# Optimization experiments

Hardware: AMD Instinct MI355X
Metric: run time of the kernel (lower is better)

The kernel has to match this reference:

```python
import jax, jax.numpy as jnp
import numpy as np

N, C, H, W = 64, 64, 8, 8   # batch, channels (img_net_out_dim), feature-map HxW
E = 256                      # ques_rnn_hidden_dim
G = 512                      # rn_g_dim
FD = 512                     # rn_f_dim
GIN = 2 * (C + 2) + E        # g-MLP input dim = 388
NUM_CLASSES = 2


def _lin(key, din, dout):
    # kaiming-uniform-like init for a Linear stored as (in, out)
    bound = float(np.sqrt(6.0 / din))
    w = jax.random.uniform(key, (din, dout), minval=-bound, maxval=bound, dtype=jnp.float32)
    b = jnp.zeros((dout,), dtype=jnp.float32)
    return w, b


def setup_inputs() -> dict:
    key = jax.random.key(0)
    ks = jax.random.split(key, 9)
    img = jax.random.normal(ks[0], (N, C, H, W), dtype=jnp.float32)
    ques = jax.random.normal(ks[1], (N, E), dtype=jnp.float32)
    g_w1, g_b1 = _lin(ks[2], GIN, G)
    g_w2, g_b2 = _lin(ks[3], G, G)
    g_w3, g_b3 = _lin(ks[4], G, G)
    g_w4, g_b4 = _lin(ks[5], G, G)
    f_w1, f_b1 = _lin(ks[6], G, FD)
    f_w2, f_b2 = _lin(ks[7], FD, FD)
    f_w3, f_b3 = _lin(ks[8], FD, NUM_CLASSES)
    return dict(img=img, ques=ques,
                g_w1=g_w1, g_b1=g_b1, g_w2=g_w2, g_b2=g_b2,
                g_w3=g_w3, g_b3=g_b3, g_w4=g_w4, g_b4=g_b4,
                f_w1=f_w1, f_b1=f_b1, f_w2=f_w2, f_b2=f_b2,
                f_w3=f_w3, f_b3=f_b3)


def _img_to_pairs(img, ques):
    # img: (n, c, h, w), ques: (n, e) -> pairs: (n, hw*hw, 2*(c+2)+e)
    n, c, h, w = img.shape
    hw = h * w
    cells = img.reshape(n, c, hw)
    idx = jnp.arange(hw)
    loc = jnp.stack([idx // w, idx % w], axis=0).astype(img.dtype)  # (2, hw)
    cells = jnp.concatenate([cells, jnp.broadcast_to(loc[None], (n, 2, hw))], axis=1)
    feats = cells.transpose(0, 2, 1)  # (n, hw, c+2)
    fdim = feats.shape[-1]
    one = jnp.broadcast_to(feats[:, :, None, :], (n, hw, hw, fdim))   # object i
    two = jnp.broadcast_to(feats[:, None, :, :], (n, hw, hw, fdim))   # object j
    q = jnp.broadcast_to(ques[:, None, None, :], (n, hw, hw, ques.shape[-1]))
    return jnp.concatenate([one, two, q], axis=-1).reshape(n, hw * hw, -1)


def reference(img, ques, g_w1, g_b1, g_w2, g_b2, g_w3, g_b3, g_w4, g_b4,
              f_w1, f_b1, f_w2, f_b2, f_w3, f_b3):
    pairs = _img_to_pairs(img, ques)                      # (N, HW^2, GIN)
    hdd = jax.nn.relu(pairs @ g_w1 + g_b1)                # shared g-MLP over all pairs
    hdd = jax.nn.relu(hdd @ g_w2 + g_b2)
    hdd = jax.nn.relu(hdd @ g_w3 + g_b3)
    hdd = jax.nn.relu(hdd @ g_w4 + g_b4)
    context = hdd.mean(axis=1)                            # (N, G)
    z = jax.nn.relu(context @ f_w1 + f_b1)                # f-MLP (dropout = identity in eval)
    z = jax.nn.relu(z @ f_w2 + f_b2)
    scores = z @ f_w3 + f_b3                              # (N, 2)
    return jax.nn.log_softmax(scores, axis=1)
```

## Files before the change

### kernel.cpp

```cpp
#include <hip/hip_runtime.h>

typedef unsigned short u16;
typedef unsigned int u32;
typedef _Float16 f16;

using half8 = __attribute__((ext_vector_type(8))) _Float16;
using f32x4 = __attribute__((ext_vector_type(4))) float;

__device__ __forceinline__ void async16(const void* g, void* l) {
    __builtin_amdgcn_global_load_lds(
        (const __attribute__((address_space(1))) u32*)g,
        (__attribute__((address_space(3))) u32*)l, 16, 0, 0);
}

__global__ __launch_bounds__(512) void prep_p12(const float* __restrict__ img,
                                                const float* __restrict__ gw1,
                                                float* __restrict__ P1,
                                                f16* __restrict__ P2h) {
    const int blk = blockIdx.x;
    const int n = blk >> 3;
    const int c0 = (blk & 7) * 8;
    const int t = threadIdx.x;
    __shared__ float feats[8][68];
    for (int idx = t; idx < 8 * 66; idx += 512) {
        int rr = idx / 66, cc = idx % 66, cell = c0 + rr;
        float v;
        if (cc < 64)       v = img[((size_t)(n * 64 + cc)) * 64 + cell];
        else if (cc == 64) v = (float)(cell >> 3);
        else               v = (float)(cell & 7);
        feats[rr][cc] = v;
    }
    __syncthreads();
    const int g = t;
    float a1[8], a2[8];
#pragma unroll
    for (int r = 0; r < 8; ++r) { a1[r] = 0.f; a2[r] = 0.f; }
    for (int c = 0; c < 66; ++c) {
        float wa = gw1[(size_t)c * 512 + g];
        float wb = gw1[(size_t)(66 + c) * 512 + g];
#pragma unroll
        for (int r = 0; r < 8; ++r) {
            a1[r] += feats[r][c] * wa;
            a2[r] += feats[r][c] * wb;
        }
    }
#pragma unroll
    for (int r = 0; r < 8; ++r) {
        P1[((size_t)(n * 64 + c0 + r)) * 512 + g] = a1[r];
        P2h[((size_t)(n * 64 + c0 + r)) * 512 + g] = (f16)a2[r];
    }
}

__global__ __launch_bounds__(512) void prep_q2(const float* __restrict__ ques,
                                               const float* __restrict__ gw1,
                                               const float* __restrict__ gb1,
                                               const float* __restrict__ P1,
                                               f16* __restrict__ P1h,
                                               float* __restrict__ Ctx) {
    const int n = blockIdx.x;
    const int t = threadIdx.x;
    __shared__ float q[256];
    if (t < 256) q[t] = ques[(size_t)n * 256 + t];
    __syncthreads();
    float acc = gb1[t];
    for (int e = 0; e < 256; ++e)
        acc += q[e] * gw1[(size_t)(132 + e) * 512 + t];
    const float* src = P1 + (((size_t)(n * 64)) << 9) + t;
    f16* dst = P1h + (((size_t)(n * 64)) << 9) + t;
    for (int r = 0; r < 64; ++r)
        dst[(size_t)r * 512] = (f16)(src[(size_t)r * 512] + acc);
    Ctx[(size_t)n * 512 + t] = 0.f;
}

__global__ void transpose_w(const float* __restrict__ W2, const float* __restrict__ W3,
                            const float* __restrict__ W4, f16* __restrict__ T2,
                            f16* __restrict__ T3, f16* __restrict__ T4) {
    const int L = blockIdx.z;
    const float* W = (L == 0) ? W2 : ((L == 1) ? W3 : W4);
    f16* T = (L == 0) ? T2 : ((L == 1) ? T3 : T4);
    __shared__ float tile[32][33];
    const int bx = blockIdx.x * 32;
    const int by = blockIdx.y * 32;
    const int tx = threadIdx.x, ty = threadIdx.y;
    for (int r = ty; r < 32; r += 8)
        tile[r][tx] = W[(size_t)(by + r) * 512 + bx + tx];
    __syncthreads();
    for (int r = ty; r < 32; r += 8)
        T[(size_t)(bx + r) * 512 + by + tx] = (f16)tile[tx][r];
}

__global__ __launch_bounds__(256, 2) void gemm2c(
    const f16* __restrict__ P1h, const f16* __restrict__ P2h,
    const f16* __restrict__ Bt, const float* __restrict__ bias,
    f16* __restrict__ Out, int row_base) {
    const int tid = threadIdx.x;
    const int lane = tid & 63;
    const int quad = lane >> 4;
    const int l15 = lane & 15;
    const int wv = tid >> 6;
    const int wm = wv >> 1, wn = wv & 1;
    const int b  = blockIdx.x;
    const int x  = b & 7;
    const int s  = b >> 3;
    const int bn = s & 3;
    const int bm = (s >> 2) * 8 + x;

    __shared__ alignas(16) f16 lA[2][256 * 32];
    __shared__ alignas(16) f16 lB[2][128 * 32];

    const int p0 = row_base + bm * 256;
    const int nb = p0 >> 12;
    const f16* P1b = P1h + (((size_t)(nb * 64)) << 9);
    const f16* P2b = P2h + (((size_t)(nb * 64)) << 9);

    auto stageB = [&](int kt, int buf) {
#pragma unroll
        for (int c = 0; c < 2; ++c) {
            int p = c * 256 + tid;
            int r = p >> 2;
            int g = ((p & 3) - (r >> 1)) & 3;
            const f16* srcB = Bt + (((size_t)(bn * 128 + r)) << 9) + kt * 32 + g * 8;
            async16(srcB, &lB[buf][(c * 256 + (tid & ~63)) * 8]);
        }
    };
    auto constructA = [&](int kt, int buf) {
#pragma unroll
        for (int c = 0; c < 4; ++c) {
            int p = c * 256 + tid;
            int r = p >> 2;
            int g = ((p & 3) - (r >> 1)) & 3;
            int k = kt * 32 + g * 8;
            int ii = ((bm * 4) + (r >> 6)) & 63;
            int jj = r & 63;
            half8 xx = *(const half8*)(P1b + (((size_t)ii) << 9) + k);
            half8 yy = *(const half8*)(P2b + (((size_t)jj) << 9) + k);
            half8 sv = xx + yy;
            sv = __builtin_elementwise_max(sv, (half8)(f16)0.f);
            *(half8*)&lA[buf][p * 8] = sv;
        }
    };

    f32x4 acc[8][4];
#pragma unroll
    for (int mi = 0; mi < 8; ++mi)
#pragma unroll
        for (int ni = 0; ni < 4; ++ni)
            acc[mi][ni] = (f32x4){0.f, 0.f, 0.f, 0.f};

    stageB(0, 0);
    constructA(0, 0);
    __syncthreads();

    for (int kt = 0; kt < 16; ++kt) {
        const int cur = kt & 1;
        if (kt < 15) {
            stageB(kt + 1, cur ^ 1);
            constructA(kt + 1, cur ^ 1);
        }
        half8 af[8], bf[4];
#pragma unroll
        for (int mi = 0; mi < 8; ++mi) {
            int r = wm * 128 + mi * 16 + l15;
            af[mi] = *(const half8*)&lA[cur][(r * 4 + ((quad + (r >> 1)) & 3)) * 8];
        }
#pragma unroll
        for (int ni = 0; ni < 4; ++ni) {
            int r = wn * 64 + ni * 16 + l15;
            bf[ni] = *(const half8*)&lB[cur][(r * 4 + ((quad + (r >> 1)) & 3)) * 8];
        }
#pragma unroll
        for (int mi = 0; mi < 8; ++mi)
#pragma unroll
            for (int ni = 0; ni < 4; ++ni)
                acc[mi][ni] = __builtin_amdgcn_mfma_f32_16x16x32_f16(
                    af[mi], bf[ni], acc[mi][ni], 0, 0, 0);
        __syncthreads();
    }

#pragma unroll
    for (int mi = 0; mi < 8; ++mi) {
#pragma unroll
        for (int ni = 0; ni < 4; ++ni) {
            int col = bn * 128 + wn * 64 + ni * 16 + l15;
            float bb = bias[col];
#pragma unroll
            for (int rr = 0; rr < 4; ++rr) {
                int row = bm * 256 + wm * 128 + mi * 16 + quad * 4 + rr;
                float v = fmaxf(acc[mi][ni][rr] + bb, 0.f);
                Out[(((size_t)row) << 9) + col] = (f16)v;
            }
        }
    }
}

template <bool REDUCE>
__global__ __launch_bounds__(256, 2) void gemm_kernel(
    const f16* __restrict__ Ain, const f16* __restrict__ Bt,
    const float* __restrict__ bias, f16* __restrict__ Out,
    float* __restrict__ Ctx, int row_base) {
    const int tid = threadIdx.x;
    const int lane = tid & 63;
    const int quad = lane >> 4;
    const int l15 = lane & 15;
    const int wv = tid >> 6;
    const int wm = wv >> 1, wn = wv & 1;
    const int b  = blockIdx.x;
    const int x  = b & 7;
    const int s  = b >> 3;
    const int bn = s & 3;
    const int bm = (s >> 2) * 8 + x;

    __shared__ alignas(16) f16 lA[256 * 64];
    __shared__ alignas(16) f16 lB[128 * 64];
    __shared__ float lsum[128];

    if (REDUCE && tid < 128) lsum[tid] = 0.f;

    f32x4 acc[8][4];
#pragma unroll
    for (int mi = 0; mi < 8; ++mi)
#pragma unroll
        for (int ni = 0; ni < 4; ++ni)
            acc[mi][ni] = (f32x4){0.f, 0.f, 0.f, 0.f};

    for (int kt = 0; kt < 8; ++kt) {
        const int k0 = kt * 64;
#pragma unroll
        for (int c = 0; c < 8; ++c) {
            int p = c * 256 + tid;
            int r = p >> 3;
            int gc = ((p & 7) - r) & 7;
            const f16* srcA = Ain + (((size_t)(bm * 256 + r)) << 9) + k0 + gc * 8;
            async16(srcA, &lA[(c * 256 + (tid & ~63)) * 8]);
        }
#pragma unroll
        for (int c = 0; c < 4; ++c) {
            int p = c * 256 + tid;
            int r = p >> 3;
            int gc = ((p & 7) - r) & 7;
            const f16* srcB = Bt + (((size_t)(bn * 128 + r)) << 9) + k0 + gc * 8;
            async16(srcB, &lB[(c * 256 + (tid & ~63)) * 8]);
        }
        __syncthreads();
#pragma unroll
        for (int ks = 0; ks < 2; ++ks) {
            half8 af[8], bf[4];
            const int gc = ks * 4 + quad;
#pragma unroll
            for (int mi = 0; mi < 8; ++mi) {
                int r = wm * 128 + mi * 16 + l15;
                af[mi] = *(const half8*)&lA[(r * 8 + ((gc + r) & 7)) * 8];
            }
#pragma unroll
            for (int ni = 0; ni < 4; ++ni) {
                int r = wn * 64 + ni * 16 + l15;
                bf[ni] = *(const half8*)&lB[(r * 8 + ((gc + r) & 7)) * 8];
            }
#pragma unroll
            for (int mi = 0; mi < 8; ++mi)
#pragma unroll
                for (int ni = 0; ni < 4; ++ni)
                    acc[mi][ni] = __builtin_amdgcn_mfma_f32_16x16x32_f16(
                        af[mi], bf[ni], acc[mi][ni], 0, 0, 0);
        }
        __syncthreads();
    }

    if (!REDUCE) {
#pragma unroll
        for (int mi = 0; mi < 8; ++mi) {
#pragma unroll
            for (int ni = 0; ni < 4; ++ni) {
                int col = bn * 128 + wn * 64 + ni * 16 + l15;
                float bb = bias[col];
#pragma unroll
                for (int rr = 0; rr < 4; ++rr) {
                    int row = bm * 256 + wm * 128 + mi * 16 + quad * 4 + rr;
                    float v = fmaxf(acc[mi][ni][rr] + bb, 0.f);
                    Out[(((size_t)row) << 9) + col] = (f16)v;
                }
            }
        }
    } else {
#pragma unroll
        for (int ni = 0; ni < 4; ++ni) {
            int coll = wn * 64 + ni * 16 + l15;
            float bb = bias[bn * 128 + coll];
            float ssum = 0.f;
#pragma unroll
            for (int mi = 0; mi < 8; ++mi)
#pragma unroll
                for (int rr = 0; rr < 4; ++rr)
                    ssum += fmaxf(acc[mi][ni][rr] + bb, 0.f);
            ssum += __shfl_xor(ssum, 16, 64);
            ssum += __shfl_xor(ssum, 32, 64);
            if (quad == 0) atomicAdd(&lsum[coll], ssum);
        }
        __syncthreads();
        if (tid < 128) {
            int nb = (row_base + bm * 256) >> 12;
            atomicAdd(&Ctx[(((size_t)nb) << 9) + bn * 128 + tid], lsum[tid]);
        }
    }
}

__global__ __launch_bounds__(512) void fmlp_layer(
    const float* __restrict__ In, const float* __restrict__ Wt,
    const float* __restrict__ bias, float* __restrict__ Out, float scale) {
    const int n = blockIdx.x, cs = blockIdx.y;
    const int t = threadIdx.x;
    const int col = cs * 64 + (t & 63);
    const int seg = t >> 6;
    __shared__ float a[512];
    __shared__ float red[512];
    a[t] = In[(size_t)n * 512 + t] * scale;
    __syncthreads();
    float p = 0.f;
#pragma unroll 8
    for (int i = seg * 64; i < seg * 64 + 64; ++i)
        p += a[i] * Wt[(size_t)i * 512 + col];
    red[t] = p;
    __syncthreads();
    if (t < 64) {
        float v = bias[col];
#pragma unroll
        for (int sg = 0; sg < 8; ++sg) v += red[sg * 64 + t];
        Out[(size_t)n * 512 + cs * 64 + t] = fmaxf(v, 0.f);
    }
}

__global__ __launch_bounds__(64) void fmlp_out(
    const float* __restrict__ A2, const float* __restrict__ fw3,
    const float* __restrict__ fb3, float* __restrict__ out) {
    const int n = blockIdx.x;
    const int lane = threadIdx.x;
    float s0 = 0.f, s1 = 0.f;
    for (int i = lane; i < 512; i += 64) {
        float v = A2[(size_t)n * 512 + i];
        s0 += v * fw3[i * 2];
        s1 += v * fw3[i * 2 + 1];
    }
#pragma unroll
    for (int d = 1; d < 64; d <<= 1) {
        s0 += __shfl_xor(s0, d, 64);
        s1 += __shfl_xor(s1, d, 64);
    }
    if (lane == 0) {
        s0 += fb3[0];
        s1 += fb3[1];
        float m = fmaxf(s0, s1);
        float l = logf(expf(s0 - m) + expf(s1 - m)) + m;
        out[n * 2 + 0] = s0 - l;
        out[n * 2 + 1] = s1 - l;
    }
}

extern "C" void kernel_launch(void* const* d_in, const int* in_sizes, int n_in,
                              void* d_out, int out_size, void* d_ws, size_t ws_size,
                              hipStream_t stream) {
    const float* img  = (const float*)d_in[0];
    const float* ques = (const float*)d_in[1];
    const float* gw1  = (const float*)d_in[2];
    const float* gb1  = (const float*)d_in[3];
    const float* gw2  = (const float*)d_in[4];
    const float* gb2  = (const float*)d_in[5];
    const float* gw3  = (const float*)d_in[6];
    const float* gb3  = (const float*)d_in[7];
    const float* gw4  = (const float*)d_in[8];
    const float* gb4  = (const float*)d_in[9];
    const float* fw1  = (const float*)d_in[10];
    const float* fb1  = (const float*)d_in[11];
    const float* fw2  = (const float*)d_in[12];
    const float* fb2  = (const float*)d_in[13];
    const float* fw3  = (const float*)d_in[14];
    const float* fb3  = (const float*)d_in[15];

    char* ws = (char*)d_ws;
    size_t off = 0;
    float* P1  = (float*)(ws + off); off += (size_t)4096 * 512 * 4;
    f16* P1h = (f16*)(ws + off); off += (size_t)4096 * 512 * 2;
    f16* P2h = (f16*)(ws + off); off += (size_t)4096 * 512 * 2;
    float* Ctx = (float*)(ws + off); off += (size_t)64 * 512 * 4;
    float* Z1  = (float*)(ws + off); off += (size_t)64 * 512 * 4;
    float* Z2  = (float*)(ws + off); off += (size_t)64 * 512 * 4;
    f16* T2 = (f16*)(ws + off); off += (size_t)512 * 512 * 2;
    f16* T3 = (f16*)(ws + off); off += (size_t)512 * 512 * 2;
    f16* T4 = (f16*)(ws + off); off += (size_t)512 * 512 * 2;
    const int MCH = 65536;
    f16* HA = (f16*)(ws + off); off += (size_t)MCH * 512 * 2;
    f16* HB = (f16*)(ws + off); off += (size_t)MCH * 512 * 2;

    prep_p12<<<512, 512, 0, stream>>>(img, gw1, P1, P2h);
    prep_q2<<<64, 512, 0, stream>>>(ques, gw1, gb1, P1, P1h, Ctx);
    transpose_w<<<dim3(16, 16, 3), dim3(32, 8), 0, stream>>>(gw2, gw3, gw4, T2, T3, T4);

    const int ggrid = (MCH / 256) * 4;
    for (int ch = 0; ch < 262144 / MCH; ++ch) {
        int row_base = ch * MCH;
        gemm2c<<<ggrid, 256, 0, stream>>>(P1h, P2h, T2, gb2, HB, row_base);
        gemm_kernel<false><<<ggrid, 256, 0, stream>>>(HB, T3, gb3, HA, nullptr, row_base);
        gemm_kernel<true ><<<ggrid, 256, 0, stream>>>(HA, T4, gb4, nullptr, Ctx, row_base);
    }

    fmlp_layer<<<dim3(64, 8), 512, 0, stream>>>(Ctx, fw1, fb1, Z1, 1.0f / 4096.0f);
    fmlp_layer<<<dim3(64, 8), 512, 0, stream>>>(Z1, fw2, fb2, Z2, 1.0f);
    fmlp_out<<<64, 64, 0, stream>>>(Z2, fw3, fb3, (float*)d_out);
}
```

Baseline: 575.9 us.

## Shrink GEMM M-tile to 128 and double-buffer K=32 stages in gemm_kernel

Halves the M tile of all three g-MLP GEMMs from 256 to 128 rows, doubles the grid, and raises the occupancy hint to 3 blocks per CU. gemm_kernel also moves from single-buffered K=64 stages to double-buffered K=32 stages, so async loads of the next tile overlap the MFMAs on the current one. The aim is more resident waves and less load latency exposed on each stage. In exchange, arithmetic intensity per tile drops, B traffic per output rises, and more atomics go to Ctx in the reduce kernel.

Result: slower. 665.1 us (+15.5%).

```diff
diff --git a/kernel.cpp b/kernel.cpp
--- a/kernel.cpp
+++ b/kernel.cpp
@@ -89,7 +89,7 @@
         T[(size_t)(bx + r) * 512 + by + tx] = (f16)tile[tx][r];
 }
 
-__global__ __launch_bounds__(256, 2) void gemm2c(
+__global__ __launch_bounds__(256, 3) void gemm2c(
     const f16* __restrict__ P1h, const f16* __restrict__ P2h,
     const f16* __restrict__ Bt, const float* __restrict__ bias,
     f16* __restrict__ Out, int row_base) {
@@ -105,10 +105,10 @@
     const int bn = s & 3;
     const int bm = (s >> 2) * 8 + x;
 
-    __shared__ alignas(16) f16 lA[2][256 * 32];
+    __shared__ alignas(16) f16 lA[2][128 * 32];
     __shared__ alignas(16) f16 lB[2][128 * 32];
 
-    const int p0 = row_base + bm * 256;
+    const int p0 = row_base + bm * 128;
     const int nb = p0 >> 12;
     const f16* P1b = P1h + (((size_t)(nb * 64)) << 9);
     const f16* P2b = P2h + (((size_t)(nb * 64)) << 9);
@@ -125,12 +125,12 @@
     };
     auto constructA = [&](int kt, int buf) {
 #pragma unroll
-        for (int c = 0; c < 4; ++c) {
+        for (int c = 0; c < 2; ++c) {
             int p = c * 256 + tid;
             int r = p >> 2;
             int g = ((p & 3) - (r >> 1)) & 3;
             int k = kt * 32 + g * 8;
-            int ii = ((bm * 4) + (r >> 6)) & 63;
+            int ii = ((bm * 2) + (r >> 6)) & 63;
             int jj = r & 63;
             half8 xx = *(const half8*)(P1b + (((size_t)ii) << 9) + k);
             half8 yy = *(const half8*)(P2b + (((size_t)jj) << 9) + k);
@@ -140,9 +140,9 @@
         }
     };
 
-    f32x4 acc[8][4];
-#pragma unroll
-    for (int mi = 0; mi < 8; ++mi)
+    f32x4 acc[4][4];
+#pragma unroll
+    for (int mi = 0; mi < 4; ++mi)
 #pragma unroll
         for (int ni = 0; ni < 4; ++ni)
             acc[mi][ni] = (f32x4){0.f, 0.f, 0.f, 0.f};
@@ -157,10 +157,10 @@
             stageB(kt + 1, cur ^ 1);
             constructA(kt + 1, cur ^ 1);
         }
-        half8 af[8], bf[4];
-#pragma unroll
-        for (int mi = 0; mi < 8; ++mi) {
-            int r = wm * 128 + mi * 16 + l15;
+        half8 af[4], bf[4];
+#pragma unroll
+        for (int mi = 0; mi < 4; ++mi) {
+            int r = wm * 64 + mi * 16 + l15;
             af[mi] = *(const half8*)&lA[cur][(r * 4 + ((quad + (r >> 1)) & 3)) * 8];
         }
 #pragma unroll
@@ -169,7 +169,7 @@
             bf[ni] = *(const half8*)&lB[cur][(r * 4 + ((quad + (r >> 1)) & 3)) * 8];
         }
 #pragma unroll
-        for (int mi = 0; mi < 8; ++mi)
+        for (int mi = 0; mi < 4; ++mi)
 #pragma unroll
             for (int ni = 0; ni < 4; ++ni)
                 acc[mi][ni] = __builtin_amdgcn_mfma_f32_16x16x32_f16(
@@ -178,14 +178,14 @@
     }
 
 #pragma unroll
-    for (int mi = 0; mi < 8; ++mi) {
+    for (int mi = 0; mi < 4; ++mi) {
 #pragma unroll
         for (int ni = 0; ni < 4; ++ni) {
             int col = bn * 128 + wn * 64 + ni * 16 + l15;
             float bb = bias[col];
 #pragma unroll
             for (int rr = 0; rr < 4; ++rr) {
-                int row = bm * 256 + wm * 128 + mi * 16 + quad * 4 + rr;
+                int row = bm * 128 + wm * 64 + mi * 16 + quad * 4 + rr;
                 float v = fmaxf(acc[mi][ni][rr] + bb, 0.f);
                 Out[(((size_t)row) << 9) + col] = (f16)v;
             }
@@ -194,7 +194,7 @@
 }
 
 template <bool REDUCE>
-__global__ __launch_bounds__(256, 2) void gemm_kernel(
+__global__ __launch_bounds__(256, 3) void gemm_kernel(
     const f16* __restrict__ Ain, const f16* __restrict__ Bt,
     const float* __restrict__ bias, f16* __restrict__ Out,
     float* __restrict__ Ctx, int row_base) {
@@ -210,72 +210,68 @@
     const int bn = s & 3;
     const int bm = (s >> 2) * 8 + x;
 
-    __shared__ alignas(16) f16 lA[256 * 64];
-    __shared__ alignas(16) f16 lB[128 * 64];
+    __shared__ alignas(16) f16 lA[2][128 * 32];
+    __shared__ alignas(16) f16 lB[2][128 * 32];
     __shared__ float lsum[128];
 
     if (REDUCE && tid < 128) lsum[tid] = 0.f;
 
-    f32x4 acc[8][4];
-#pragma unroll
-    for (int mi = 0; mi < 8; ++mi)
+    auto stageAB = [&](int kt, int buf) {
+#pragma unroll
+        for (int c = 0; c < 2; ++c) {
+            int p = c * 256 + tid;
+            int r = p >> 2;
+            int g = ((p & 3) - (r >> 1)) & 3;
+            const f16* srcA = Ain + (((size_t)(bm * 128 + r)) << 9) + kt * 32 + g * 8;
+            async16(srcA, &lA[buf][(c * 256 + (tid & ~63)) * 8]);
+            const f16* srcB = Bt + (((size_t)(bn * 128 + r)) << 9) + kt * 32 + g * 8;
+            async16(srcB, &lB[buf][(c * 256 + (tid & ~63)) * 8]);
+        }
+    };
+
+    f32x4 acc[4][4];
+#pragma unroll
+    for (int mi = 0; mi < 4; ++mi)
 #pragma unroll
         for (int ni = 0; ni < 4; ++ni)
             acc[mi][ni] = (f32x4){0.f, 0.f, 0.f, 0.f};
 
-    for (int kt = 0; kt < 8; ++kt) {
-        const int k0 = kt * 64;
-#pragma unroll
-        for (int c = 0; c < 8; ++c) {
-            int p = c * 256 + tid;
-            int r = p >> 3;
-            int gc = ((p & 7) - r) & 7;
-            const f16* srcA = Ain + (((size_t)(bm * 256 + r)) << 9) + k0 + gc * 8;
-            async16(srcA, &lA[(c * 256 + (tid & ~63)) * 8]);
-        }
-#pragma unroll
-        for (int c = 0; c < 4; ++c) {
-            int p = c * 256 + tid;
-            int r = p >> 3;
-            int gc = ((p & 7) - r) & 7;
-            const f16* srcB = Bt + (((size_t)(bn * 128 + r)) << 9) + k0 + gc * 8;
-            async16(srcB, &lB[(c * 256 + (tid & ~63)) * 8]);
-        }
+    stageAB(0, 0);
+    __syncthreads();
+
+    for (int kt = 0; kt < 16; ++kt) {
+        const int cur = kt & 1;
+        if (kt < 15) stageAB(kt + 1, cur ^ 1);
+        half8 af[4], bf[4];
+#pragma unroll
+        for (int mi = 0; mi < 4; ++mi) {
+            int r = wm * 64 + mi * 16 + l15;
+            af[mi] = *(const half8*)&lA[cur][(r * 4 + ((quad + (r >> 1)) & 3)) * 8];
+        }
+#pragma unroll
+        for (int ni = 0; ni < 4; ++ni) {
+            int r = wn * 64 + ni * 16 + l15;
+            bf[ni] = *(const half8*)&lB[cur][(r * 4 + ((quad + (r >> 1)) & 3)) * 8];
+        }
+#pragma unroll
+        for (int mi = 0; mi < 4; ++mi)
+#pragma unroll
+            for (int ni = 0; ni < 4; ++ni)
+                acc[mi][ni] = __builtin_amdgcn_mfma_f32_16x16x32_f16(
+                    af[mi], bf[ni], acc[mi][ni], 0, 0, 0);
         __syncthreads();
-#pragma unroll
-        for (int ks = 0; ks < 2; ++ks) {
-            half8 af[8], bf[4];
-            const int gc = ks * 4 + quad;
-#pragma unroll
-            for (int mi = 0; mi < 8; ++mi) {
-                int r = wm * 128 + mi * 16 + l15;
-                af[mi] = *(const half8*)&lA[(r * 8 + ((gc + r) & 7)) * 8];
-            }
-#pragma unroll
-            for (int ni = 0; ni < 4; ++ni) {
-                int r = wn * 64 + ni * 16 + l15;
-                bf[ni] = *(const half8*)&lB[(r * 8 + ((gc + r) & 7)) * 8];
-            }
-#pragma unroll
-            for (int mi = 0; mi < 8; ++mi)
-#pragma unroll
-                for (int ni = 0; ni < 4; ++ni)
-                    acc[mi][ni] = __builtin_amdgcn_mfma_f32_16x16x32_f16(
-                        af[mi], bf[ni], acc[mi][ni], 0, 0, 0);
-        }
-        __syncthreads();
     }
 
     if (!REDUCE) {
 #pragma unroll
-        for (int mi = 0; mi < 8; ++mi) {
+        for (int mi = 0; mi < 4; ++mi) {
 #pragma unroll
             for (int ni = 0; ni < 4; ++ni) {
                 int col = bn * 128 + wn * 64 + ni * 16 + l15;
                 float bb = bias[col];
 #pragma unroll
                 for (int rr = 0; rr < 4; ++rr) {
-                    int row = bm * 256 + wm * 128 + mi * 16 + quad * 4 + rr;
+                    int row = bm * 128 + wm * 64 + mi * 16 + quad * 4 + rr;
                     float v = fmaxf(acc[mi][ni][rr] + bb, 0.f);
                     Out[(((size_t)row) << 9) + col] = (f16)v;
                 }
@@ -288,7 +284,7 @@
             float bb = bias[bn * 128 + coll];
             float ssum = 0.f;
 #pragma unroll
-            for (int mi = 0; mi < 8; ++mi)
+            for (int mi = 0; mi < 4; ++mi)
 #pragma unroll
                 for (int rr = 0; rr < 4; ++rr)
                     ssum += fmaxf(acc[mi][ni][rr] + bb, 0.f);
@@ -298,7 +294,7 @@
         }
         __syncthreads();
         if (tid < 128) {
-            int nb = (row_base + bm * 256) >> 12;
+            int nb = (row_base + bm * 128) >> 12;
             atomicAdd(&Ctx[(((size_t)nb) << 9) + bn * 128 + tid], lsum[tid]);
         }
     }
@@ -394,7 +390,7 @@
     prep_q2<<<64, 512, 0, stream>>>(ques, gw1, gb1, P1, P1h, Ctx);
     transpose_w<<<dim3(16, 16, 3), dim3(32, 8), 0, stream>>>(gw2, gw3, gw4, T2, T3, T4);
 
-    const int ggrid = (MCH / 256) * 4;
+    const int ggrid = (MCH / 128) * 4;
     for (int ch = 0; ch < 262144 / MCH; ++ch) {
         int row_base = ch * MCH;
         gemm2c<<<ggrid, 256, 0, stream>>>(P1h, P2h, T2, gb2, HB, row_base);
```

## Double-buffer GEMM LDS tiles with K=32 stages to overlap loads and MFMA

Applied to the files above, without the earlier changes.

Splits the K loop into 16 stages of 32 instead of 8 stages of 64, and keeps two LDS buffers for A and B. The next stage is issued through async global-to-LDS loads while MFMAs run on the current buffer, which is meant to hide memory latency behind compute. The swizzle changes to a 4-chunk row pattern keyed on r>>1. The cost is one barrier per smaller stage and less work between barriers. There is also a possible hazard: it depends on the async LDS writes being complete when the single barrier per iteration is reached.

New measurement: 682.5 us. 18.5% more time.

```diff
diff --git a/kernel.cpp b/kernel.cpp
--- a/kernel.cpp
+++ b/kernel.cpp
@@ -210,11 +210,30 @@
     const int bn = s & 3;
     const int bm = (s >> 2) * 8 + x;
 
-    __shared__ alignas(16) f16 lA[256 * 64];
-    __shared__ alignas(16) f16 lB[128 * 64];
+    __shared__ alignas(16) f16 lA[2][256 * 32];
+    __shared__ alignas(16) f16 lB[2][128 * 32];
     __shared__ float lsum[128];
 
     if (REDUCE && tid < 128) lsum[tid] = 0.f;
+
+    auto stageAB = [&](int kt, int buf) {
+#pragma unroll
+        for (int c = 0; c < 4; ++c) {
+            int p = c * 256 + tid;
+            int r = p >> 2;
+            int g = ((p & 3) - (r >> 1)) & 3;
+            const f16* srcA = Ain + (((size_t)(bm * 256 + r)) << 9) + kt * 32 + g * 8;
+            async16(srcA, &lA[buf][(c * 256 + (tid & ~63)) * 8]);
+        }
+#pragma unroll
+        for (int c = 0; c < 2; ++c) {
+            int p = c * 256 + tid;
+            int r = p >> 2;
+            int g = ((p & 3) - (r >> 1)) & 3;
+            const f16* srcB = Bt + (((size_t)(bn * 128 + r)) << 9) + kt * 32 + g * 8;
+            async16(srcB, &lB[buf][(c * 256 + (tid & ~63)) * 8]);
+        }
+    };
 
     f32x4 acc[8][4];
 #pragma unroll
@@ -223,46 +242,29 @@
         for (int ni = 0; ni < 4; ++ni)
             acc[mi][ni] = (f32x4){0.f, 0.f, 0.f, 0.f};
 
-    for (int kt = 0; kt < 8; ++kt) {
-        const int k0 = kt * 64;
-#pragma unroll
-        for (int c = 0; c < 8; ++c) {
-            int p = c * 256 + tid;
-            int r = p >> 3;
-            int gc = ((p & 7) - r) & 7;
-            const f16* srcA = Ain + (((size_t)(bm * 256 + r)) << 9) + k0 + gc * 8;
-            async16(srcA, &lA[(c * 256 + (tid & ~63)) * 8]);
-        }
-#pragma unroll
-        for (int c = 0; c < 4; ++c) {
-            int p = c * 256 + tid;
-            int r = p >> 3;
-            int gc = ((p & 7) - r) & 7;
-            const f16* srcB = Bt + (((size_t)(bn * 128 + r)) << 9) + k0 + gc * 8;
-            async16(srcB, &lB[(c * 256 + (tid & ~63)) * 8]);
-        }
-        __syncthreads();
-#pragma unroll
-        for (int ks = 0; ks < 2; ++ks) {
-            half8 af[8], bf[4];
-            const int gc = ks * 4 + quad;
-#pragma unroll
-            for (int mi = 0; mi < 8; ++mi) {
-                int r = wm * 128 + mi * 16 + l15;
-                af[mi] = *(const half8*)&lA[(r * 8 + ((gc + r) & 7)) * 8];
-            }
-#pragma unroll
-            for (int ni = 0; ni < 4; ++ni) {
-                int r = wn * 64 + ni * 16 + l15;
-                bf[ni] = *(const half8*)&lB[(r * 8 + ((gc + r) & 7)) * 8];
-            }
-#pragma unroll
-            for (int mi = 0; mi < 8; ++mi)
-#pragma unroll
-                for (int ni = 0; ni < 4; ++ni)
-                    acc[mi][ni] = __builtin_amdgcn_mfma_f32_16x16x32_f16(
-                        af[mi], bf[ni], acc[mi][ni], 0, 0, 0);
-        }
+    stageAB(0, 0);
+    __syncthreads();
+
+    for (int kt = 0; kt < 16; ++kt) {
+        const int cur = kt & 1;
+        if (kt < 15) stageAB(kt + 1, cur ^ 1);
+        half8 af[8], bf[4];
+#pragma unroll
+        for (int mi = 0; mi < 8; ++mi) {
+            int r = wm * 128 + mi * 16 + l15;
+            af[mi] = *(const half8*)&lA[cur][(r * 4 + ((quad + (r >> 1)) & 3)) * 8];
+        }
+#pragma unroll
+        for (int ni = 0; ni < 4; ++ni) {
+            int r = wn * 64 + ni * 16 + l15;
+            bf[ni] = *(const half8*)&lB[cur][(r * 4 + ((quad + (r >> 1)) & 3)) * 8];
+        }
+#pragma unroll
+        for (int mi = 0; mi < 8; ++mi)
+#pragma unroll
+            for (int ni = 0; ni < 4; ++ni)
+                acc[mi][ni] = __builtin_amdgcn_mfma_f32_16x16x32_f16(
+                    af[mi], bf[ni], acc[mi][ni], 0, 0, 0);
         __syncthreads();
     }
 
```
